# Performance work log

Measured on AMD Instinct MI355X. Metric: run time of the kernel, lower is better.

The kernel has to match this reference:

```python
import jax, jax.numpy as jnp
import numpy as np

N0, N1, N2 = 300000, 60000, 6000
E1, E2 = 1200000, 300000
R, D_IN, D_H, D_OUT = 4, 128, 128, 64
HBUF = 30000
BN_EPS = 1e-5


def setup_inputs() -> dict:
    key = jax.random.key(0)
    ks = jax.random.split(key, 16)
    inp = {
        "x": jax.random.normal(ks[0], (N0, D_IN), jnp.float32),
        "src1": jax.random.randint(ks[1], (E1,), 0, N0, jnp.int32),
        "dst1": jax.random.randint(ks[2], (E1,), 0, N1, jnp.int32),
        "et1": jax.random.randint(ks[3], (E1,), 0, R, jnp.int32),
        "src2": jax.random.randint(ks[4], (E2,), 0, N1, jnp.int32),
        "dst2": jax.random.randint(ks[5], (E2,), 0, N2, jnp.int32),
        "et2": jax.random.randint(ks[6], (E2,), 0, R, jnp.int32),
        # history_map values in [-1, HBUF-1); -1 means "no cached history"
        "history_map": jax.random.randint(ks[7], (N1,), 0, HBUF, jnp.int32) - 1,
        "history_buffer": jax.random.normal(ks[8], (HBUF, D_H), jnp.float32),
        "W1": jax.random.normal(ks[9], (R, D_IN, D_H), jnp.float32) / np.sqrt(D_IN),
        "Wself1": jax.random.normal(ks[10], (D_IN, D_H), jnp.float32) / np.sqrt(D_IN),
        "b1": jnp.zeros((D_H,), jnp.float32),
        "gamma": jnp.ones((D_H,), jnp.float32),
        "beta": jnp.zeros((D_H,), jnp.float32),
        "W2": jax.random.normal(ks[11], (R, D_H, D_OUT), jnp.float32) / np.sqrt(D_H),
        "Wself2": jax.random.normal(ks[12], (D_H, D_OUT), jnp.float32) / np.sqrt(D_H),
        "b2": jnp.zeros((D_OUT,), jnp.float32),
    }
    return inp


def relgraphconv(x, src, dst, et, n_out, W, Wself, b):
    # per-relation transform of all src nodes: [R, N, out]
    xW = jnp.einsum('ni,rio->rno', x, W)
    msg = xW[et, src]                                   # [E, out] gather
    agg = jax.ops.segment_sum(msg, dst, num_segments=n_out)  # scatter-add
    # DGL block: dst nodes are the first n_out src nodes (self loop)
    return agg + x[:n_out] @ Wself + b


def reference(x, src1, dst1, et1, src2, dst2, et2, history_map,
              history_buffer, W1, Wself1, b1, gamma, beta, W2, Wself2, b2):
    # layer 1: RGCN + history overwrite
    h = relgraphconv(x, src1, dst1, et1, N1, W1, Wself1, b1)
    valid = history_map >= 0
    safe_idx = jnp.where(valid, history_map, 0)
    h = jnp.where(valid[:, None], history_buffer[safe_idx], h)
    # BatchNorm1d (training: batch statistics), relu; dropout p=0.0
    mean = jnp.mean(h, axis=0)
    var = jnp.var(h, axis=0)
    h = (h - mean) * jax.lax.rsqrt(var + BN_EPS) * gamma + beta
    h = jax.nn.relu(h)
    # layer 2: RGCN (history_size=0 path), log-softmax
    out = relgraphconv(h, src2, dst2, et2, N2, W2, Wself2, b2)
    return jax.nn.log_softmax(out, axis=-1)
```

## Files before the change

kernel.cpp:

```cpp
#include <hip/hip_runtime.h>
#include <hip/hip_bf16.h>

#define N0 300000
#define N1 60000
#define N2 6000
#define E1 1200000
#define E2 300000
#define D 128
#define DO 64
#define HBUF 30000

#define WL_CAP 32768
#define UC_CAP 256
#define CAP 192

#define CONV_BLKS 469
#define ESCAN_BLKS 4688
#define BFRAG_BLKS 160

typedef __attribute__((ext_vector_type(8))) short bfrag8;
typedef __attribute__((ext_vector_type(4))) float f32x4;

__device__ __forceinline__ float bf2f(unsigned int u) {
    union { unsigned int i; float f; } c; c.i = u << 16; return c.f;
}
__device__ __forceinline__ unsigned short f2bf(float f) {
    return __bfloat16_as_ushort(__float2bfloat16(f));
}

__global__ void k_zero(float* __restrict__ hfix, int* __restrict__ mcount,
                       int* __restrict__ degcnt, int* __restrict__ cnt,
                       int* __restrict__ nuc) {
    int i = blockIdx.x * 256 + threadIdx.x;
    int stride = gridDim.x * 256;
    for (int j = i; j < UC_CAP * D; j += stride) hfix[j] = 0.f;
    for (int j = i; j < HBUF; j += stride) mcount[j] = 0;
    for (int j = i; j < N2 * 16; j += stride) degcnt[j] = 0;
    if (i == 0) { *cnt = 0; *nuc = 0; }
}

__global__ void k_scan(const int* __restrict__ hmap, int* __restrict__ mcount,
                       int* __restrict__ nuc, int* __restrict__ uc_node,
                       int* __restrict__ remap) {
    int node = blockIdx.x * 256 + threadIdx.x;
    if (node >= N1) return;
    int m = hmap[node];
    if (m >= 0) {
        atomicAdd(&mcount[m], 1);
        remap[node] = m;
    } else {
        int slot = atomicAdd(nuc, 1);
        if (slot > UC_CAP - 1) slot = UC_CAP - 1;
        uc_node[slot] = node;
        remap[node] = HBUF + slot;
    }
}

__global__ void __launch_bounds__(256) k_A(
        const float* __restrict__ hist, unsigned short* __restrict__ histbf,
        const int* __restrict__ mcount, float* __restrict__ psum,
        const int* __restrict__ hmap, const int* __restrict__ remap,
        const int* __restrict__ dst1, int* __restrict__ cnt, int* __restrict__ list,
        const int* __restrict__ src2, const int* __restrict__ dst2,
        const int* __restrict__ et2, int* __restrict__ degcnt,
        int* __restrict__ epay,
        const float* __restrict__ W2, const float* __restrict__ Wself2,
        unsigned short* __restrict__ BF) {
    int b = blockIdx.x, tid = threadIdx.x;
    if (b < CONV_BLKS) {
        __shared__ float ls1[2048], ls2[2048];
        float s[8] = {0,0,0,0,0,0,0,0}, ss[8] = {0,0,0,0,0,0,0,0};
        const float4* h4 = (const float4*)hist;
#pragma unroll
        for (int it = 0; it < 4; it++) {
            int i = (b * 4 + it) * 256 + tid;
            if (i >= 480000) break;
            int row = i >> 4;
            float w = (float)mcount[row];
            float4 u = h4[(size_t)i * 2], v = h4[(size_t)i * 2 + 1];
            float e[8] = {u.x, u.y, u.z, u.w, v.x, v.y, v.z, v.w};
            union { unsigned short q[8]; uint4 o; } o;
#pragma unroll
            for (int j = 0; j < 8; j++) {
                o.q[j] = f2bf(e[j]);
                s[j] += w * e[j];
                ss[j] += w * e[j] * e[j];
            }
            *(uint4*)(histbf + (size_t)i * 8) = o.o;
        }
#pragma unroll
        for (int j = 0; j < 8; j++) { ls1[tid * 8 + j] = s[j]; ls2[tid * 8 + j] = ss[j]; }
        __syncthreads();
        if (tid < 128) {
            int qq = tid >> 3, jj = tid & 7;
            float S = 0.f, SS = 0.f;
#pragma unroll
            for (int g = 0; g < 16; g++) {
                int src = (qq + 16 * g) * 8 + jj;
                S += ls1[src]; SS += ls2[src];
            }
            psum[b * 256 + tid] = S;
            psum[b * 256 + 128 + tid] = SS;
        }
    } else if (b < CONV_BLKS + ESCAN_BLKS) {
        int e = (b - CONV_BLKS) * 256 + tid;
        if (e < E2) {
            int d = dst2[e];
            int pos = atomicAdd(&degcnt[d * 16], 1);
            if (pos < CAP) epay[d * CAP + pos] = remap[src2[e]] | (et2[e] << 16);
        }
        if (e < E1 && hmap[dst1[e]] < 0) {
            int i = atomicAdd(cnt, 1);
            if (i < WL_CAP) list[i] = e;
        }
    } else {
        int idx = (b - CONV_BLKS - ESCAN_BLKS) * 256 + tid;
        int j = idx & 7, lane = (idx >> 3) & 63, sub = (idx >> 9) & 15, g = idx >> 13;
        int kt = sub >> 2, ct = sub & 3;
        int k = kt * 32 + (lane >> 4) * 8 + j;
        int col = ct * 16 + (lane & 15);
        float v = (g < 4) ? W2[(g * D + k) * DO + col] : Wself2[k * DO + col];
        BF[idx] = f2bf(v);
    }
}

__global__ void __launch_bounds__(256) k_wl2(
        const float* __restrict__ x, const int* __restrict__ src1,
        const int* __restrict__ dst1, const int* __restrict__ et1,
        const float* __restrict__ W1, const float* __restrict__ Wself1,
        const float* __restrict__ b1, const int* __restrict__ cnt,
        const int* __restrict__ list, const int* __restrict__ remap,
        const int* __restrict__ uc_node, const int* __restrict__ nuc,
        float* __restrict__ hfix, const float* __restrict__ psum,
        float* __restrict__ psum2) {
    int b = blockIdx.x, tid = threadIdx.x;
    if (b < 16) {
        int c = tid & 127, half = tid >> 7;
        int n = *cnt; if (n > WL_CAP) n = WL_CAP;
        for (int i = b * 2 + half; i < n; i += 32) {
            int e = list[i];
            int s = src1[e], d = dst1[e], t = et1[e];
            int slot = remap[d] - HBUF;
            if (slot < 0 || slot >= UC_CAP) continue;
            float acc = 0.f;
            for (int k = 0; k < D; k++) acc += x[(size_t)s * D + k] * W1[(t * D + k) * D + c];
            atomicAdd(&hfix[slot * D + c], acc);
        }
    } else if (b < 24) {
        int n = *nuc; if (n > UC_CAP) n = UC_CAP;
        int c = tid & 127, half = tid >> 7;
        for (int slot = (b - 16) * 2 + half; slot < n; slot += 16) {
            int node = uc_node[slot];
            float acc = b1[c];
            for (int k = 0; k < D; k++) acc += x[(size_t)node * D + k] * Wself1[k * D + c];
            atomicAdd(&hfix[slot * D + c], acc);
        }
    } else {
        int r = b - 24;
        float S = 0.f;
        for (int i = r; i < CONV_BLKS; i += 16) S += psum[i * 256 + tid];
        psum2[r * 256 + tid] = S;
    }
}

__global__ void k_mid(const float* __restrict__ psum2, const float* __restrict__ hfix,
                      const int* __restrict__ nuc,
                      const float* __restrict__ gamma, const float* __restrict__ beta,
                      float* __restrict__ params,
                      unsigned short* __restrict__ histbf) {
    int b = blockIdx.x, tid = threadIdx.x;
    if (b == 0) {
        if (tid < 128) {
            float S = 0.f, SS = 0.f;
#pragma unroll
            for (int r = 0; r < 16; r++) {
                S += psum2[r * 256 + tid];
                SS += psum2[r * 256 + 128 + tid];
            }
            int n = *nuc; if (n > UC_CAP) n = UC_CAP;
            for (int slot = 0; slot < n; slot++) {
                float v = hfix[slot * D + tid];
                S += v; SS += v * v;
            }
            float mean = S / (float)N1;
            float var = SS / (float)N1 - mean * mean;
            float sc = gamma[tid] * rsqrtf(var + 1e-5f);
            params[tid] = sc;
            params[128 + tid] = beta[tid] - mean * sc;
        }
    } else {
        for (int i = tid; i < UC_CAP * D; i += 256)
            histbf[(size_t)HBUF * D + i] = f2bf(hfix[i]);
    }
}

#define AGG_ACC(P, V) { \
    int t_ = (P) >> 16; \
    float f0_ = fmaxf(bf2f((V) & 0xffff) * sc0 + sh0, 0.f); \
    float f1_ = fmaxf(bf2f((V) >> 16) * sc1 + sh1, 0.f); \
    acc[0][0] += (t_ == 0) ? f0_ : 0.f; acc[0][1] += (t_ == 0) ? f1_ : 0.f; \
    acc[1][0] += (t_ == 1) ? f0_ : 0.f; acc[1][1] += (t_ == 1) ? f1_ : 0.f; \
    acc[2][0] += (t_ == 2) ? f0_ : 0.f; acc[2][1] += (t_ == 2) ? f1_ : 0.f; \
    acc[3][0] += (t_ == 3) ? f0_ : 0.f; acc[3][1] += (t_ == 3) ? f1_ : 0.f; }

__global__ void __launch_bounds__(256) k_agg(const unsigned int* __restrict__ hbu,
                                             const int* __restrict__ degcnt,
                                             const int* __restrict__ epay,
                                             const float* __restrict__ params,
                                             unsigned int* __restrict__ aggbu) {
    __shared__ float red[4 * 4 * 128];
    int d = blockIdx.x;
    int wave = threadIdx.x >> 6, lane = threadIdx.x & 63;
    float sc0 = params[2 * lane],     sh0 = params[128 + 2 * lane];
    float sc1 = params[2 * lane + 1], sh1 = params[128 + 2 * lane + 1];
    float acc[4][2] = {};
    int j1 = degcnt[d * 16]; if (j1 > CAP) j1 = CAP;
    const int* ep = epay + d * CAP;
    int j = wave;
    for (; j + 12 < j1; j += 16) {
        int p0 = ep[j], p1 = ep[j + 4], p2 = ep[j + 8], p3 = ep[j + 12];
        unsigned int v0 = hbu[(size_t)(p0 & 0xffff) * 64 + lane];
        unsigned int v1 = hbu[(size_t)(p1 & 0xffff) * 64 + lane];
        unsigned int v2 = hbu[(size_t)(p2 & 0xffff) * 64 + lane];
        unsigned int v3 = hbu[(size_t)(p3 & 0xffff) * 64 + lane];
        AGG_ACC(p0, v0); AGG_ACC(p1, v1); AGG_ACC(p2, v2); AGG_ACC(p3, v3);
    }
    for (; j < j1; j += 4) {
        int p = ep[j];
        unsigned int v = hbu[(size_t)(p & 0xffff) * 64 + lane];
        AGG_ACC(p, v);
    }
#pragma unroll
    for (int t = 0; t < 4; t++) {
        red[(wave * 4 + t) * 128 + 2 * lane]     = acc[t][0];
        red[(wave * 4 + t) * 128 + 2 * lane + 1] = acc[t][1];
    }
    __syncthreads();
    int t = threadIdx.x >> 6, l2 = threadIdx.x & 63;
    float s0 = 0.f, s1 = 0.f;
#pragma unroll
    for (int w = 0; w < 4; w++) {
        s0 += red[(w * 4 + t) * 128 + 2 * l2];
        s1 += red[(w * 4 + t) * 128 + 2 * l2 + 1];
    }
    aggbu[((size_t)t * N2 + d) * 64 + l2] =
        (unsigned int)f2bf(s0) | ((unsigned int)f2bf(s1) << 16);
}

__global__ void __launch_bounds__(256) k_gemm2(const unsigned short* __restrict__ aggb,
                                               const unsigned short* __restrict__ histbf,
                                               const int* __restrict__ remap,
                                               const unsigned short* __restrict__ BF,
                                               const float* __restrict__ params,
                                               const float* __restrict__ b2,
                                               float* __restrict__ out) {
    int row0 = blockIdx.x * 64;
    int wave = threadIdx.x >> 6, lane = threadIdx.x & 63;
    int r = row0 + wave * 16 + (lane & 15);
    int rl = (r < N2) ? r : N2 - 1;
    int ridx = remap[rl];
    int kb = (lane >> 4) * 8;
    f32x4 acc[4] = {};
#pragma unroll
    for (int kt = 0; kt < 4; kt++) {
#pragma unroll
        for (int g = 0; g < 5; g++) {
            bfrag8 a;
            if (g < 4) {
                a = *reinterpret_cast<const bfrag8*>(aggb + ((size_t)(g * N2 + rl) * D + kt * 32 + kb));
            } else {
                bfrag8 raw = *reinterpret_cast<const bfrag8*>(histbf + ((size_t)ridx * D + kt * 32 + kb));
#pragma unroll
                for (int j = 0; j < 8; j++) {
                    int c = kt * 32 + kb + j;
                    float f = bf2f((unsigned int)(unsigned short)raw[j]);
                    f = fmaxf(f * params[c] + params[128 + c], 0.f);
                    a[j] = (short)f2bf(f);
                }
            }
#pragma unroll
            for (int ct = 0; ct < 4; ct++) {
                bfrag8 bb = *reinterpret_cast<const bfrag8*>(BF + ((((g * 4 + kt) * 4 + ct) * 64 + lane) * 8));
                acc[ct] = __builtin_amdgcn_mfma_f32_16x16x32_bf16(a, bb, acc[ct], 0, 0, 0);
            }
        }
    }
    float bb4[4];
#pragma unroll
    for (int ct = 0; ct < 4; ct++) bb4[ct] = b2[ct * 16 + (lane & 15)];
    int srow = row0 + wave * 16 + (lane >> 4) * 4;
#pragma unroll
    for (int i = 0; i < 4; i++) {
        float v[4];
#pragma unroll
        for (int ct = 0; ct < 4; ct++) v[ct] = acc[ct][i] + bb4[ct];
        float m = fmaxf(fmaxf(v[0], v[1]), fmaxf(v[2], v[3]));
#pragma unroll
        for (int sh = 1; sh <= 8; sh <<= 1) m = fmaxf(m, __shfl_xor(m, sh, 64));
        float s = 0.f;
#pragma unroll
        for (int ct = 0; ct < 4; ct++) s += expf(v[ct] - m);
#pragma unroll
        for (int sh = 1; sh <= 8; sh <<= 1) s += __shfl_xor(s, sh, 64);
        float lg = m + logf(s);
        int rr = srow + i;
        if (rr < N2) {
#pragma unroll
            for (int ct = 0; ct < 4; ct++)
                out[(size_t)rr * DO + ct * 16 + (lane & 15)] = v[ct] - lg;
        }
    }
}

extern "C" void kernel_launch(void* const* d_in, const int* in_sizes, int n_in,
                              void* d_out, int out_size, void* d_ws, size_t ws_size,
                              hipStream_t stream) {
    const float* x      = (const float*)d_in[0];
    const int* src1     = (const int*)d_in[1];
    const int* dst1     = (const int*)d_in[2];
    const int* et1      = (const int*)d_in[3];
    const int* src2     = (const int*)d_in[4];
    const int* dst2     = (const int*)d_in[5];
    const int* et2      = (const int*)d_in[6];
    const int* hmap     = (const int*)d_in[7];
    const float* hist   = (const float*)d_in[8];
    const float* W1     = (const float*)d_in[9];
    const float* Wself1 = (const float*)d_in[10];
    const float* b1     = (const float*)d_in[11];
    const float* gamma  = (const float*)d_in[12];
    const float* beta   = (const float*)d_in[13];
    const float* W2     = (const float*)d_in[14];
    const float* Wself2 = (const float*)d_in[15];
    const float* b2     = (const float*)d_in[16];
    float* out = (float*)d_out;

    char* ws = (char*)d_ws;
    unsigned short* histbf = (unsigned short*)(ws);
    unsigned short* aggb   = (unsigned short*)(ws + 7745536);
    unsigned short* BF     = (unsigned short*)(ws + 13889536);
    float* hfix            = (float*)(ws + 13971456);
    int* uc_node           = (int*)(ws + 14102528);
    int* remap             = (int*)(ws + 14103552);
    int* epay              = (int*)(ws + 14343552);
    int* mcount            = (int*)(ws + 18951552);
    int* degcnt            = (int*)(ws + 19071552);
    float* psum            = (float*)(ws + 19455552);
    float* psum2           = (float*)(ws + 19935808);
    int* list              = (int*)(ws + 19952192);
    float* params          = (float*)(ws + 20083264);
    int* cnt               = (int*)(ws + 20084288);
    int* nuc               = (int*)(ws + 20084292);

    k_zero<<<128, 256, 0, stream>>>(hfix, mcount, degcnt, cnt, nuc);
    k_scan<<<(N1 + 255) / 256, 256, 0, stream>>>(hmap, mcount, nuc, uc_node, remap);
    k_A<<<CONV_BLKS + ESCAN_BLKS + BFRAG_BLKS, 256, 0, stream>>>(
        hist, histbf, mcount, psum, hmap, remap,
        dst1, cnt, list, src2, dst2, et2, degcnt, epay, W2, Wself2, BF);
    k_wl2<<<40, 256, 0, stream>>>(x, src1, dst1, et1, W1, Wself1, b1,
                                  cnt, list, remap, uc_node, nuc,
                                  hfix, psum, psum2);
    k_mid<<<2, 256, 0, stream>>>(psum2, hfix, nuc, gamma, beta, params, histbf);
    k_agg<<<N2, 256, 0, stream>>>((const unsigned int*)histbf, degcnt, epay,
                                  params, (unsigned int*)aggb);
    k_gemm2<<<94, 256, 0, stream>>>(aggb, histbf, remap, BF, params, b2, out);
}
```

Measured before the change: 98.93 us.

## Widen worklist parallelism, move BN stat reduction into k_mid, batch agg gathers

The worklist layer-1 fix-up kernel now uses 64 blocks instead of 16 for edge messages, and its inner dot-product loops get an unroll hint. The psum partial reduction moves out of k_wl2 into k_mid, where each of 128 blocks reduces one channel with a shared-memory tree, replacing a single block that serialised the final reduction. k_agg gives each wave a contiguous chunk of edges and issues 16 clamped gathers before accumulating, to increase memory-level parallelism. The cost is higher register pressure in k_agg and redundant clamped loads on tail iterations.

```diff
diff --git a/kernel.cpp b/kernel.cpp
--- a/kernel.cpp
+++ b/kernel.cpp
@@ -131,62 +131,66 @@
         const float* __restrict__ b1, const int* __restrict__ cnt,
         const int* __restrict__ list, const int* __restrict__ remap,
         const int* __restrict__ uc_node, const int* __restrict__ nuc,
-        float* __restrict__ hfix, const float* __restrict__ psum,
-        float* __restrict__ psum2) {
+        float* __restrict__ hfix) {
     int b = blockIdx.x, tid = threadIdx.x;
-    if (b < 16) {
+    if (b < 64) {
         int c = tid & 127, half = tid >> 7;
         int n = *cnt; if (n > WL_CAP) n = WL_CAP;
-        for (int i = b * 2 + half; i < n; i += 32) {
+        for (int i = b * 2 + half; i < n; i += 128) {
             int e = list[i];
             int s = src1[e], d = dst1[e], t = et1[e];
             int slot = remap[d] - HBUF;
             if (slot < 0 || slot >= UC_CAP) continue;
             float acc = 0.f;
+#pragma unroll 4
             for (int k = 0; k < D; k++) acc += x[(size_t)s * D + k] * W1[(t * D + k) * D + c];
             atomicAdd(&hfix[slot * D + c], acc);
         }
-    } else if (b < 24) {
+    } else {
         int n = *nuc; if (n > UC_CAP) n = UC_CAP;
         int c = tid & 127, half = tid >> 7;
-        for (int slot = (b - 16) * 2 + half; slot < n; slot += 16) {
+        for (int slot = (b - 64) * 2 + half; slot < n; slot += 16) {
             int node = uc_node[slot];
             float acc = b1[c];
+#pragma unroll 4
             for (int k = 0; k < D; k++) acc += x[(size_t)node * D + k] * Wself1[k * D + c];
             atomicAdd(&hfix[slot * D + c], acc);
         }
-    } else {
-        int r = b - 24;
-        float S = 0.f;
-        for (int i = r; i < CONV_BLKS; i += 16) S += psum[i * 256 + tid];
-        psum2[r * 256 + tid] = S;
-    }
-}
-
-__global__ void k_mid(const float* __restrict__ psum2, const float* __restrict__ hfix,
-                      const int* __restrict__ nuc,
-                      const float* __restrict__ gamma, const float* __restrict__ beta,
-                      float* __restrict__ params,
-                      unsigned short* __restrict__ histbf) {
+    }
+}
+
+__global__ void __launch_bounds__(256) k_mid(
+        const float* __restrict__ psum, const float* __restrict__ hfix,
+        const int* __restrict__ nuc,
+        const float* __restrict__ gamma, const float* __restrict__ beta,
+        float* __restrict__ params, unsigned short* __restrict__ histbf) {
     int b = blockIdx.x, tid = threadIdx.x;
-    if (b == 0) {
-        if (tid < 128) {
-            float S = 0.f, SS = 0.f;
-#pragma unroll
-            for (int r = 0; r < 16; r++) {
-                S += psum2[r * 256 + tid];
-                SS += psum2[r * 256 + 128 + tid];
-            }
-            int n = *nuc; if (n > UC_CAP) n = UC_CAP;
-            for (int slot = 0; slot < n; slot++) {
-                float v = hfix[slot * D + tid];
-                S += v; SS += v * v;
-            }
-            float mean = S / (float)N1;
-            float var = SS / (float)N1 - mean * mean;
-            float sc = gamma[tid] * rsqrtf(var + 1e-5f);
-            params[tid] = sc;
-            params[128 + tid] = beta[tid] - mean * sc;
+    if (b < 128) {
+        int c = b;
+        __shared__ float r1[256], r2[256];
+        float S = 0.f, SS = 0.f;
+        for (int r = tid; r < CONV_BLKS; r += 256) {
+            S += psum[r * 256 + c];
+            SS += psum[r * 256 + 128 + c];
+        }
+        r1[tid] = S; r2[tid] = SS;
+        __syncthreads();
+        for (int off = 128; off; off >>= 1) {
+            if (tid < off) { r1[tid] += r1[tid + off]; r2[tid] += r2[tid + off]; }
+            __syncthreads();
+        }
+        if (tid == 0) {
+            float Sf = r1[0], SSf = r2[0];
+            int nn = *nuc; if (nn > UC_CAP) nn = UC_CAP;
+            for (int slot = 0; slot < nn; slot++) {
+                float v = hfix[slot * D + c];
+                Sf += v; SSf += v * v;
+            }
+            float mean = Sf / (float)N1;
+            float var = SSf / (float)N1 - mean * mean;
+            float sc = gamma[c] * rsqrtf(var + 1e-5f);
+            params[c] = sc;
+            params[128 + c] = beta[c] - mean * sc;
         }
     } else {
         for (int i = tid; i < UC_CAP * D; i += 256)
@@ -214,21 +218,26 @@
     float sc0 = params[2 * lane],     sh0 = params[128 + 2 * lane];
     float sc1 = params[2 * lane + 1], sh1 = params[128 + 2 * lane + 1];
     float acc[4][2] = {};
-    int j1 = degcnt[d * 16]; if (j1 > CAP) j1 = CAP;
+    int n = degcnt[d * 16]; if (n > CAP) n = CAP;
     const int* ep = epay + d * CAP;
-    int j = wave;
-    for (; j + 12 < j1; j += 16) {
-        int p0 = ep[j], p1 = ep[j + 4], p2 = ep[j + 8], p3 = ep[j + 12];
-        unsigned int v0 = hbu[(size_t)(p0 & 0xffff) * 64 + lane];
-        unsigned int v1 = hbu[(size_t)(p1 & 0xffff) * 64 + lane];
-        unsigned int v2 = hbu[(size_t)(p2 & 0xffff) * 64 + lane];
-        unsigned int v3 = hbu[(size_t)(p3 & 0xffff) * 64 + lane];
-        AGG_ACC(p0, v0); AGG_ACC(p1, v1); AGG_ACC(p2, v2); AGG_ACC(p3, v3);
-    }
-    for (; j < j1; j += 4) {
-        int p = ep[j];
-        unsigned int v = hbu[(size_t)(p & 0xffff) * 64 + lane];
-        AGG_ACC(p, v);
+    int chunk = (n + 3) >> 2;
+    int s0 = wave * chunk;
+    int s1 = s0 + chunk; if (s1 > n) s1 = n;
+    for (int base = s0; base < s1; base += 16) {
+        int last = s1 - 1;
+        int p[16]; unsigned int v[16];
+#pragma unroll
+        for (int q = 0; q < 16; q++) {
+            int idx = base + q;
+            p[q] = ep[idx <= last ? idx : last];
+        }
+#pragma unroll
+        for (int q = 0; q < 16; q++)
+            v[q] = hbu[(size_t)(p[q] & 0xffff) * 64 + lane];
+#pragma unroll
+        for (int q = 0; q < 16; q++) {
+            if (base + q <= last) { AGG_ACC(p[q], v[q]); }
+        }
     }
 #pragma unroll
     for (int t = 0; t < 4; t++) {
@@ -237,14 +246,14 @@
     }
     __syncthreads();
     int t = threadIdx.x >> 6, l2 = threadIdx.x & 63;
-    float s0 = 0.f, s1 = 0.f;
+    float s0f = 0.f, s1f = 0.f;
 #pragma unroll
     for (int w = 0; w < 4; w++) {
-        s0 += red[(w * 4 + t) * 128 + 2 * l2];
-        s1 += red[(w * 4 + t) * 128 + 2 * l2 + 1];
+        s0f += red[(w * 4 + t) * 128 + 2 * l2];
+        s1f += red[(w * 4 + t) * 128 + 2 * l2 + 1];
     }
     aggbu[((size_t)t * N2 + d) * 64 + l2] =
-        (unsigned int)f2bf(s0) | ((unsigned int)f2bf(s1) << 16);
+        (unsigned int)f2bf(s0f) | ((unsigned int)f2bf(s1f) << 16);
 }
 
 __global__ void __launch_bounds__(256) k_gemm2(const unsigned short* __restrict__ aggb,
@@ -345,7 +354,6 @@
     int* mcount            = (int*)(ws + 18951552);
     int* degcnt            = (int*)(ws + 19071552);
     float* psum            = (float*)(ws + 19455552);
-    float* psum2           = (float*)(ws + 19935808);
     int* list              = (int*)(ws + 19952192);
     float* params          = (float*)(ws + 20083264);
     int* cnt               = (int*)(ws + 20084288);
@@ -356,10 +364,9 @@
     k_A<<<CONV_BLKS + ESCAN_BLKS + BFRAG_BLKS, 256, 0, stream>>>(
         hist, histbf, mcount, psum, hmap, remap,
         dst1, cnt, list, src2, dst2, et2, degcnt, epay, W2, Wself2, BF);
-    k_wl2<<<40, 256, 0, stream>>>(x, src1, dst1, et1, W1, Wself1, b1,
-                                  cnt, list, remap, uc_node, nuc,
-                                  hfix, psum, psum2);
-    k_mid<<<2, 256, 0, stream>>>(psum2, hfix, nuc, gamma, beta, params, histbf);
+    k_wl2<<<72, 256, 0, stream>>>(x, src1, dst1, et1, W1, Wself1, b1,
+                                  cnt, list, remap, uc_node, nuc, hfix);
+    k_mid<<<129, 256, 0, stream>>>(psum, hfix, nuc, gamma, beta, params, histbf);
     k_agg<<<N2, 256, 0, stream>>>((const unsigned int*)histbf, degcnt, epay,
                                   params, (unsigned int*)aggb);
     k_gemm2<<<94, 256, 0, stream>>>(aggb, histbf, remap, BF, params, b2, out);
```

Measured after the change: 95.59 us. -3.4%, faster.
